# Kernel optimization log

Hardware: AMD Instinct MI355X
Metric: run time of the kernel (lower is better)

Reference implementation:

```python
import jax, jax.numpy as jnp
import numpy as np

B, N, H, W, P = 32, 6, 512, 512, 512
SCALE, ASPECT, MIN_PH = 0.5, 1.0, 60.0


def setup_inputs() -> dict:
    key = jax.random.key(0)
    k1, k2, k3, k4, k5, k6 = jax.random.split(key, 6)
    images = jax.random.normal(k1, (B, H, W, 3), jnp.float32)
    patch = jax.random.normal(k2, (P, P, 3), jnp.float32)
    # person bboxes (ymin, xmin, ymax, xmax) in pixels, fully inside the image
    hsz = jax.random.uniform(k3, (B, N), jnp.float32, 120.0, 400.0)
    wsz = jax.random.uniform(k4, (B, N), jnp.float32, 120.0, 400.0)
    ymin = jax.random.uniform(k5, (B, N), jnp.float32) * (H - hsz)
    xmin = jax.random.uniform(k6, (B, N), jnp.float32) * (W - wsz)
    boxes = jnp.stack([ymin, xmin, ymin + hsz, xmin + wsz], axis=-1)
    return {"images": images, "boxes": boxes, "patch": patch}


def _patch_boxes(boxes):
    # Patcher.create: derive (ymin_patch, xmin_patch, patch_h, patch_w) from each bbox
    ymin, xmin, ymax, xmax = (boxes[..., 0], boxes[..., 1], boxes[..., 2], boxes[..., 3])
    h = ymax - ymin
    w = xmax - xmin
    pw = h * SCALE
    ph = ASPECT * pw
    oy = ymin + h * 0.5
    ox = xmin + w * 0.5
    yp = jnp.maximum(oy - ph * 0.5, 0.0)
    xp = jnp.maximum(ox - pw * 0.5, 0.0)
    yp = jnp.where(yp + ph > H, H - ph, yp)
    xp = jnp.where(xp + pw > W, W - pw, xp)
    valid = ph > MIN_PH  # ragged filter -> mask
    return jnp.stack([yp, xp, ph, pw], axis=-1), valid


def _paste_one(img, patch, box, valid):
    # fused gather(resize bilinear, half-pixel centers) + scatter of the patch into img
    Pn = patch.shape[0]
    b = box.astype(jnp.int32)  # tf.cast truncation
    y0b, x0b, h, w = b[0], b[1], b[2], b[3]
    hf = jnp.maximum(h, 1).astype(jnp.float32)
    wf = jnp.maximum(w, 1).astype(jnp.float32)
    dy = jnp.arange(img.shape[0]) - y0b
    dx = jnp.arange(img.shape[1]) - x0b
    sy = jnp.clip((dy.astype(jnp.float32) + 0.5) * (Pn / hf) - 0.5, 0.0, Pn - 1.0)
    sx = jnp.clip((dx.astype(jnp.float32) + 0.5) * (Pn / wf) - 0.5, 0.0, Pn - 1.0)
    yl = jnp.floor(sy).astype(jnp.int32); yh = jnp.minimum(yl + 1, Pn - 1); wy = sy - yl
    xl = jnp.floor(sx).astype(jnp.int32); xh = jnp.minimum(xl + 1, Pn - 1); wx = sx - xl
    # separable bilinear: rows [H, P, 3] then cols -> [H, W, 3]
    rows = patch[yl] * (1.0 - wy)[:, None, None] + patch[yh] * wy[:, None, None]
    val = rows[:, xl] * (1.0 - wx)[None, :, None] + rows[:, xh] * wx[None, :, None]
    inside = ((dy >= 0) & (dy < h))[:, None] & ((dx >= 0) & (dx < w))[None, :] & valid
    return jnp.where(inside[..., None], val, img)


def reference(images, boxes, patch):
    pboxes, valid = _patch_boxes(boxes)
    def step(imgs, xs):
        bx, v = xs  # [B,4], [B]
        imgs = jax.vmap(lambda im, b_, v_: _paste_one(im, patch, b_, v_))(imgs, bx, v)
        return imgs, None
    # sequential over patches (later patches overwrite earlier, as in the tf while_loop)
    out, _ = jax.lax.scan(step, images, (jnp.transpose(pboxes, (1, 0, 2)), valid.T))
    return out
```

## Files before the change

### kernel.cpp

```cpp
#include <hip/hip_runtime.h>


#define Nn 6
#define Hh 512
#define Ww 512
#define Pp 512

__global__ __launch_bounds__(256) void patch_attack_kernel(
    const float* __restrict__ images,
    const float* __restrict__ boxes,
    const float* __restrict__ patch,
    float* __restrict__ out)
{
    __shared__ int   s_y0[Nn], s_x0[Nn], s_h[Nn], s_w[Nn];
    __shared__ float s_sy[Nn], s_sx[Nn];

    const int b = blockIdx.x >> 10;

    if (threadIdx.x < Nn) {
        const int n = threadIdx.x;
        const float* bx = boxes + ((size_t)b * Nn + n) * 4;
        const float ymin = bx[0], xmin = bx[1], ymax = bx[2], xmax = bx[3];
        const float h  = ymax - ymin;
        const float w  = xmax - xmin;
        const float pw = h * 0.5f;
        const float ph = pw;
        const float oy = ymin + h * 0.5f;
        const float ox = xmin + w * 0.5f;
        float yp = fmaxf(oy - ph * 0.5f, 0.0f);
        float xp = fmaxf(ox - pw * 0.5f, 0.0f);
        yp = (yp + ph > 512.0f) ? (512.0f - ph) : yp;
        xp = (xp + pw > 512.0f) ? (512.0f - pw) : xp;
        const bool valid = ph > 60.0f;
        const int hI = (int)ph;
        const int wI = (int)pw;
        s_y0[n] = (int)yp;
        s_x0[n] = (int)xp;
        s_h[n]  = valid ? hI : 0;
        s_w[n]  = wI;
        s_sy[n] = 512.0f / (float)(hI > 1 ? hI : 1);
        s_sx[n] = 512.0f / (float)(wI > 1 ? wI : 1);
    }
    __syncthreads();

    int   y0[Nn], x0[Nn], hh[Nn], ww[Nn];
    float syv[Nn], sxv[Nn];
    #pragma unroll
    for (int n = 0; n < Nn; ++n) {
        y0[n]  = s_y0[n];
        x0[n]  = s_x0[n];
        hh[n]  = s_h[n];
        ww[n]  = s_w[n];
        syv[n] = s_sy[n];
        sxv[n] = s_sx[n];
    }

    const int pix = blockIdx.x * 256 + threadIdx.x;
    const int rem = pix & (Hh * Ww - 1);
    const int y   = rem >> 9;
    const int x   = rem & (Ww - 1);

    float r0, r1, r2;
    bool covered = false;

    #pragma unroll
    for (int n = Nn - 1; n >= 0; --n) {
        const int dy = y - y0[n];
        const int dx = x - x0[n];
        if ((unsigned)dy < (unsigned)hh[n] && (unsigned)dx < (unsigned)ww[n]) {
            float sy = ((float)dy + 0.5f) * syv[n] - 0.5f;
            float sx = ((float)dx + 0.5f) * sxv[n] - 0.5f;
            sy = fminf(fmaxf(sy, 0.0f), 511.0f);
            sx = fminf(fmaxf(sx, 0.0f), 511.0f);
            const int yl = (int)sy;
            const int yh = (yl + 1 < 511) ? (yl + 1) : 511;
            const float wy = sy - (float)yl;
            const int xl = (int)sx;
            const int xh = (xl + 1 < 511) ? (xl + 1) : 511;
            const float wx = sx - (float)xl;
            const float omwy = 1.0f - wy;
            const float omwx = 1.0f - wx;

            const float* __restrict__ pll = patch + ((size_t)yl * Pp + xl) * 3;
            const float* __restrict__ plh = patch + ((size_t)yl * Pp + xh) * 3;
            const float* __restrict__ phl = patch + ((size_t)yh * Pp + xl) * 3;
            const float* __restrict__ phh = patch + ((size_t)yh * Pp + xh) * 3;
            r0 = (pll[0] * omwy + phl[0] * wy) * omwx + (plh[0] * omwy + phh[0] * wy) * wx;
            r1 = (pll[1] * omwy + phl[1] * wy) * omwx + (plh[1] * omwy + phh[1] * wy) * wx;
            r2 = (pll[2] * omwy + phl[2] * wy) * omwx + (plh[2] * omwy + phh[2] * wy) * wx;
            covered = true;
            break;
        }
    }

    if (!covered) {
        const float* __restrict__ ip = images + (size_t)pix * 3;
        r0 = ip[0];
        r1 = ip[1];
        r2 = ip[2];
    }

    float* __restrict__ op = out + (size_t)pix * 3;
    op[0] = r0;
    op[1] = r1;
    op[2] = r2;
}

extern "C" void kernel_launch(void* const* d_in, const int* in_sizes, int n_in,
                              void* d_out, int out_size, void* d_ws, size_t ws_size,
                              hipStream_t stream) {
    const float* images = (const float*)d_in[0];
    const float* boxes  = (const float*)d_in[1];
    const float* patch  = (const float*)d_in[2];
    float* out = (float*)d_out;

    const int total_pixels = 32 * Hh * Ww;
    const int block = 256;
    const int grid  = total_pixels / block;

    patch_attack_kernel<<<grid, block, 0, stream>>>(images, boxes, patch, out);
}
```

Baseline: 190.8 us.

## Stage results in LDS and emit vectorized nontemporal float4 image loads/stores

Each thread now writes its RGB result and a coverage flag into shared memory. After a barrier, 192 threads each load and store one contiguous float4 of the block's 768 floats, using nontemporal loads and stores. The image load is skipped only when all four floats are covered by a patch. This replaces the per-thread stride-3 scalar global accesses with coalesced 16-byte transactions, at the cost of an extra barrier, shared-memory traffic and 64 idle threads in the final phase. The per-thread register copies of the box parameters are also dropped in favor of reading them straight from shared memory.

```diff
diff --git a/kernel.cpp b/kernel.cpp
--- a/kernel.cpp
+++ b/kernel.cpp
@@ -5,6 +5,8 @@
 #define Hh 512
 #define Ww 512
 #define Pp 512
+
+typedef float v4f __attribute__((ext_vector_type(4)));
 
 __global__ __launch_bounds__(256) void patch_attack_kernel(
     const float* __restrict__ images,
@@ -14,11 +16,14 @@
 {
     __shared__ int   s_y0[Nn], s_x0[Nn], s_h[Nn], s_w[Nn];
     __shared__ float s_sy[Nn], s_sx[Nn];
+    __shared__ float s_res[256 * 3];
+    __shared__ unsigned char s_cov[256];
 
+    const int tid = threadIdx.x;
     const int b = blockIdx.x >> 10;
 
-    if (threadIdx.x < Nn) {
-        const int n = threadIdx.x;
+    if (tid < Nn) {
+        const int n = tid;
         const float* bx = boxes + ((size_t)b * Nn + n) * 4;
         const float ymin = bx[0], xmin = bx[1], ymax = bx[2], xmax = bx[3];
         const float h  = ymax - ymin;
@@ -43,33 +48,21 @@
     }
     __syncthreads();
 
-    int   y0[Nn], x0[Nn], hh[Nn], ww[Nn];
-    float syv[Nn], sxv[Nn];
-    #pragma unroll
-    for (int n = 0; n < Nn; ++n) {
-        y0[n]  = s_y0[n];
-        x0[n]  = s_x0[n];
-        hh[n]  = s_h[n];
-        ww[n]  = s_w[n];
-        syv[n] = s_sy[n];
-        sxv[n] = s_sx[n];
-    }
-
-    const int pix = blockIdx.x * 256 + threadIdx.x;
+    const int pix = blockIdx.x * 256 + tid;
     const int rem = pix & (Hh * Ww - 1);
     const int y   = rem >> 9;
     const int x   = rem & (Ww - 1);
 
-    float r0, r1, r2;
+    float r0 = 0.0f, r1 = 0.0f, r2 = 0.0f;
     bool covered = false;
 
     #pragma unroll
     for (int n = Nn - 1; n >= 0; --n) {
-        const int dy = y - y0[n];
-        const int dx = x - x0[n];
-        if ((unsigned)dy < (unsigned)hh[n] && (unsigned)dx < (unsigned)ww[n]) {
-            float sy = ((float)dy + 0.5f) * syv[n] - 0.5f;
-            float sx = ((float)dx + 0.5f) * sxv[n] - 0.5f;
+        const int dy = y - s_y0[n];
+        const int dx = x - s_x0[n];
+        if ((unsigned)dy < (unsigned)s_h[n] && (unsigned)dx < (unsigned)s_w[n]) {
+            float sy = ((float)dy + 0.5f) * s_sy[n] - 0.5f;
+            float sx = ((float)dx + 0.5f) * s_sx[n] - 0.5f;
             sy = fminf(fmaxf(sy, 0.0f), 511.0f);
             sx = fminf(fmaxf(sx, 0.0f), 511.0f);
             const int yl = (int)sy;
@@ -93,17 +86,30 @@
         }
     }
 
-    if (!covered) {
-        const float* __restrict__ ip = images + (size_t)pix * 3;
-        r0 = ip[0];
-        r1 = ip[1];
-        r2 = ip[2];
+    s_res[tid * 3 + 0] = r0;
+    s_res[tid * 3 + 1] = r1;
+    s_res[tid * 3 + 2] = r2;
+    s_cov[tid] = covered ? 1 : 0;
+    __syncthreads();
+
+    if (tid < 192) {
+        const int f0 = tid << 2;
+        const size_t gf = (size_t)blockIdx.x * 768 + f0;
+        const bool c0 = s_cov[(f0 + 0) / 3];
+        const bool c1 = s_cov[(f0 + 1) / 3];
+        const bool c2 = s_cov[(f0 + 2) / 3];
+        const bool c3 = s_cov[(f0 + 3) / 3];
+        v4f v = {0.0f, 0.0f, 0.0f, 0.0f};
+        if (!(c0 && c1 && c2 && c3)) {
+            v = __builtin_nontemporal_load((const v4f*)(images + gf));
+        }
+        v4f o;
+        o.x = c0 ? s_res[f0 + 0] : v.x;
+        o.y = c1 ? s_res[f0 + 1] : v.y;
+        o.z = c2 ? s_res[f0 + 2] : v.z;
+        o.w = c3 ? s_res[f0 + 3] : v.w;
+        __builtin_nontemporal_store(o, (v4f*)(out + gf));
     }
-
-    float* __restrict__ op = out + (size_t)pix * 3;
-    op[0] = r0;
-    op[1] = r1;
-    op[2] = r2;
 }
 
 extern "C" void kernel_launch(void* const* d_in, const int* in_sizes, int n_in,
```

Result: no change. 190.7 us (-0.1%).
